# Optimization experiments

Measured on AMD Instinct MI355X. Metric: run time of the kernel, lower is better.

## Reference

```python
import jax, jax.numpy as jnp
import numpy as np

# dims: batch, seqlen, d_model, d_inner=2*d_model, d_state, dt_rank=ceil(dm/16), n_layer, vocab, d_conv
B_, L_, DM, DI, N, RK, NL, V, K = 2, 2048, 512, 1024, 16, 32, 4, 32000, 4


def setup_inputs() -> dict:
    key = jax.random.key(0)
    ks = jax.random.split(key, 10)
    s = lambda k, shape, scale: jax.random.normal(k, shape, jnp.float32) * scale
    return {
        "input_ids": jax.random.randint(ks[0], (B_, L_), 0, V),
        "emb": s(ks[1], (V, DM), 0.02),
        "in_proj_w": s(ks[2], (NL, 2 * DI, DM), DM ** -0.5),
        "conv_w": s(ks[3], (NL, DI, K), 0.2),
        "conv_b": jnp.zeros((NL, DI), jnp.float32),
        "x_proj_w": s(ks[4], (NL, RK + 2 * N, DI), DI ** -0.5),
        "dt_proj_w": s(ks[5], (NL, DI, RK), RK ** -0.5),
        "dt_proj_b": jnp.full((NL, DI), -4.6, jnp.float32),  # softplus^-1(~0.01)
        "A_log": jnp.tile(jnp.log(jnp.arange(1, N + 1, dtype=jnp.float32))[None, None, :], (NL, DI, 1)),
        "Dp": jnp.ones((NL, DI), jnp.float32),
        "out_proj_w": s(ks[6], (NL, DM, DI), DI ** -0.5),
        "norm_w": jnp.ones((NL, DM), jnp.float32),
        "norm_b": jnp.zeros((NL, DM), jnp.float32),
        "normf_w": jnp.ones((DM,), jnp.float32),
        "normf_b": jnp.zeros((DM,), jnp.float32),
        "dec_w": s(ks[7], (V, DM), DM ** -0.5),
        "dec_b": jnp.zeros((V,), jnp.float32),
    }


def layer_norm(x, w, b, eps=1e-5):
    m = x.mean(-1, keepdims=True)
    v = ((x - m) ** 2).mean(-1, keepdims=True)
    return (x - m) * jax.lax.rsqrt(v + eps) * w + b


def mamba_mixer(x, iw, cw, cb, xw, dw, db, A_log, Dv, ow):
    B, L, _ = x.shape
    xz = x @ iw.T                      # [B,L,2*DI]
    u, z = jnp.split(xz, 2, -1)
    # depthwise causal conv1d, kernel K
    up = jnp.pad(u, ((0, 0), (K - 1, 0), (0, 0)))
    u = sum(up[:, k:k + L, :] * cw[:, k] for k in range(K)) + cb
    u = jax.nn.silu(u)
    xdbl = u @ xw.T                    # [B,L,RK+2N]
    dt, Bm, Cm = jnp.split(xdbl, [RK, RK + N], -1)
    dt = jax.nn.softplus(dt @ dw.T + db)   # [B,L,DI]
    A = -jnp.exp(A_log)                    # [DI,N]
    dA = jnp.exp(dt[..., None] * A)                              # [B,L,DI,N]
    dBu = dt[..., None] * Bm[:, :, None, :] * u[..., None]       # [B,L,DI,N]

    def step(h, inp):
        dA_t, dBu_t, C_t = inp
        h = dA_t * h + dBu_t
        return h, jnp.einsum('bdn,bn->bd', h, C_t)

    h0 = jnp.zeros((B, DI, N), x.dtype)
    _, ys = jax.lax.scan(step, h0, (dA.transpose(1, 0, 2, 3), dBu.transpose(1, 0, 2, 3), Cm.transpose(1, 0, 2)))
    y = ys.transpose(1, 0, 2) + u * Dv
    y = y * jax.nn.silu(z)
    return y @ ow.T


def reference(input_ids, emb, in_proj_w, conv_w, conv_b, x_proj_w, dt_proj_w, dt_proj_b,
              A_log, Dp, out_proj_w, norm_w, norm_b, normf_w, normf_b, dec_w, dec_b):
    h = emb[input_ids]                 # [B,L,DM]
    residual = None
    for i in range(NL):
        residual = h + residual if residual is not None else h
        hn = layer_norm(residual, norm_w[i], norm_b[i])
        h = mamba_mixer(hn, in_proj_w[i], conv_w[i], conv_b[i], x_proj_w[i],
                        dt_proj_w[i], dt_proj_b[i], A_log[i], Dp[i], out_proj_w[i])
    residual = h + residual
    h = layer_norm(residual, normf_w, normf_b)
    return h @ dec_w.T + dec_b         # [B,L,V]
```

## Files before the change

kernel.cpp:

```cpp
#include <hip/hip_runtime.h>
#include <cstdint>
#include <cstddef>

typedef unsigned short u16;
typedef __attribute__((ext_vector_type(8))) short short8;
typedef __attribute__((ext_vector_type(4))) float f32x4;
typedef __attribute__((ext_vector_type(4))) unsigned short us4;

#define NB 2
#define SEQ 2048
#define DMODEL 512
#define DINNER 1024
#define NSTATE 16
#define RKK 32
#define NLAYER 4
#define VOCAB 32000
#define KCONV 4
#define MROWS 4096
#define NCHUNK 64
#define LCHUNK 32
#define XP_SPLITK 8
#define XP_KCH 128

#define GLOAD16(gp, lp) __builtin_amdgcn_global_load_lds( \
    (const __attribute__((address_space(1))) void*)(gp),  \
    (__attribute__((address_space(3))) void*)(lp), 16, 0, 0)

static __device__ __forceinline__ u16 f2bf(float f) {
  union { float f; uint32_t u; } v; v.f = f;
  uint32_t r = (v.u + 0x7FFFu + ((v.u >> 16) & 1u)) >> 16;
  return (u16)r;
}
static __device__ __forceinline__ float bf2f(u16 x) {
  union { uint32_t u; float f; } v; v.u = ((uint32_t)x) << 16; return v.f;
}

__global__ __launch_bounds__(256) void cvt_bf16_k(const float* __restrict__ s, u16* __restrict__ d, long n) {
  long i = ((long)blockIdx.x * 256 + threadIdx.x) * 4;
  if (i < n) {
    f32x4 v = *(const f32x4*)(s + i);
    us4 o; o.x = f2bf(v.x); o.y = f2bf(v.y); o.z = f2bf(v.z); o.w = f2bf(v.w);
    *(us4*)(d + i) = o;
  }
}
__global__ __launch_bounds__(256) void cvt_xproj_k(const float* __restrict__ s, u16* __restrict__ d) {
  long i = (long)blockIdx.x * 256 + threadIdx.x;
  int c = (int)(i & 1023); int r = ((int)(i >> 10)) & 127; int l = (int)(i >> 17);
  d[i] = (r < 64) ? f2bf(s[((long)l * 64 + r) * 1024 + c]) : (u16)0;
}

__global__ __launch_bounds__(256) void embed_k(const int* __restrict__ ids, const float* __restrict__ emb,
                        float* __restrict__ resid) {
  long gid = (long)blockIdx.x * 256 + threadIdx.x;
  int m = (int)(gid >> 9), c = (int)(gid & 511);
  resid[gid] = emb[(long)ids[m] * DMODEL + c];
}

__global__ __launch_bounds__(256) void ln_k(float* __restrict__ resid, const float* __restrict__ hadd,
                                            const float* __restrict__ w, const float* __restrict__ b,
                                            u16* __restrict__ obf) {
  int m = blockIdx.x, t = threadIdx.x;
  long base = (long)m * DMODEL;
  float x0 = resid[base + t], x1 = resid[base + t + 256];
  if (hadd) {
    x0 += hadd[base + t]; x1 += hadd[base + t + 256];
    resid[base + t] = x0; resid[base + t + 256] = x1;
  }
  float s = x0 + x1, q = x0 * x0 + x1 * x1;
  #pragma unroll
  for (int o = 1; o < 64; o <<= 1) { s += __shfl_xor(s, o, 64); q += __shfl_xor(q, o, 64); }
  __shared__ float ss[4], qq[4];
  int wv = t >> 6;
  if ((t & 63) == 0) { ss[wv] = s; qq[wv] = q; }
  __syncthreads();
  s = ss[0] + ss[1] + ss[2] + ss[3];
  q = qq[0] + qq[1] + qq[2] + qq[3];
  float mean = s * (1.f / DMODEL);
  float var = q * (1.f / DMODEL) - mean * mean;
  float rs = rsqrtf(var + 1e-5f);
  obf[base + t]       = f2bf((x0 - mean) * rs * w[t] + b[t]);
  obf[base + t + 256] = f2bf((x1 - mean) * rs * w[t + 256] + b[t + 256]);
}

__global__ __launch_bounds__(256) void conv_silu_k(const float* __restrict__ xz, const float* __restrict__ cw,
                            const float* __restrict__ cb, u16* __restrict__ ub) {
  int tid = blockIdx.x * 256 + threadIdx.x;
  int d = tid & (DINNER - 1);
  int g = tid >> 10;
  int m0 = g << 2;
  int t0 = m0 & (SEQ - 1);
  float w0 = cw[d * 4 + 0], w1 = cw[d * 4 + 1], w2 = cw[d * 4 + 2], w3 = cw[d * 4 + 3];
  float bias = cb[d];
  float v[7];
  #pragma unroll
  for (int j = 0; j < 7; ++j) {
    int tt = t0 + j - 3;
    v[j] = (tt >= 0) ? xz[(long)(m0 + j - 3) * (2 * DINNER) + d] : 0.f;
  }
  #pragma unroll
  for (int i = 0; i < 4; ++i) {
    float acc = bias + v[i] * w0 + v[i + 1] * w1 + v[i + 2] * w2 + v[i + 3] * w3;
    float sv = acc / (1.f + __expf(-acc));
    ub[(long)(m0 + i) * DINNER + d] = f2bf(sv);
  }
}

template <int EPI, bool SPLIT>
__global__ __launch_bounds__(256) void gemm_bf16(
    const u16* __restrict__ A, int lda, const u16* __restrict__ W, int ldw,
    float* __restrict__ C, u16* __restrict__ Cb, int ldc,
    const float* __restrict__ bias, int K, int kchunk, long zstride) {
  const int tid = threadIdx.x;
  const int nwg = gridDim.x * gridDim.y;
  const int wgid = blockIdx.y * gridDim.x + blockIdx.x;
  const int q = nwg >> 3;
  const int swz = (wgid & 7) * q + (wgid >> 3);
  const int bn = swz % gridDim.x, bm = swz / gridDim.x;
  int kb = 0, ke = K;
  if (SPLIT) { kb = blockIdx.z * kchunk; ke = kb + kchunk; C += (long)blockIdx.z * zstride; }
  const int wave = tid >> 6, lane = tid & 63;
  const int wm = (wave >> 1) * 64, wn = (wave & 1) * 64;
  __shared__ __align__(16) u16 sA[128 * 32];
  __shared__ __align__(16) u16 sB[128 * 32];
  f32x4 acc[4][4] = {};
  const long arow0 = (long)bm * 128, brow0 = (long)bn * 128;
  const int frow = lane & 15, fk = (lane >> 4) << 3;
  const int srow = lane >> 2, scol = (lane & 3) << 3;
  const int c0 = wave * 2;
  for (int k0 = kb; k0 < ke; k0 += 32) {
    __syncthreads();
    #pragma unroll
    for (int i = 0; i < 2; ++i) {
      int c = c0 + i;
      GLOAD16(A + (arow0 + 16 * c + srow) * (long)lda + k0 + scol, sA + c * 512);
      GLOAD16(W + (brow0 + 16 * c + srow) * (long)ldw + k0 + scol, sB + c * 512);
    }
    asm volatile("s_waitcnt vmcnt(0)" ::: "memory");
    __syncthreads();
    short8 aF[4], bF[4];
    #pragma unroll
    for (int i = 0; i < 4; ++i) aF[i] = *(const short8*)(sA + (wm + i * 16 + frow) * 32 + fk);
    #pragma unroll
    for (int i = 0; i < 4; ++i) bF[i] = *(const short8*)(sB + (wn + i * 16 + frow) * 32 + fk);
    #pragma unroll
    for (int mi = 0; mi < 4; ++mi)
      #pragma unroll
      for (int ni = 0; ni < 4; ++ni)
        acc[mi][ni] = __builtin_amdgcn_mfma_f32_16x16x32_bf16(aF[mi], bF[ni], acc[mi][ni], 0, 0, 0);
  }
  const int ccol = lane & 15, crow = (lane >> 4) << 2;
  #pragma unroll
  for (int mi = 0; mi < 4; ++mi) {
    #pragma unroll
    for (int ni = 0; ni < 4; ++ni) {
      long gr0 = arow0 + wm + mi * 16 + crow;
      long gc = brow0 + wn + ni * 16 + ccol;
      #pragma unroll
      for (int r = 0; r < 4; ++r) {
        float v = acc[mi][ni][r];
        long idx = (gr0 + r) * (long)ldc + gc;
        if (EPI == 0) {
          C[idx] = v;
        } else if (EPI == 1) {
          C[idx] = v; Cb[idx] = f2bf(v);
        } else if (EPI == 2) {
          float x = v + bias[gc];
          Cb[idx] = f2bf((x > 20.f) ? x : log1pf(__expf(x)));
        } else {
          C[idx] = v + bias[gc];
        }
      }
    }
  }
}

__global__ __launch_bounds__(256) void xp_comb_k(const float* __restrict__ P, float* __restrict__ xd,
                          u16* __restrict__ xdb) {
  long i = (long)blockIdx.x * 256 + threadIdx.x;
  float s = 0.f;
  #pragma unroll
  for (int z = 0; z < XP_SPLITK; ++z) s += P[(long)z * MROWS * 128 + i];
  xd[i] = s; xdb[i] = f2bf(s);
}

__global__ __launch_bounds__(256) void scanA_k(const u16* __restrict__ dtb, const u16* __restrict__ ubf,
                        const float* __restrict__ xd, const float* __restrict__ alog_l,
                        float* __restrict__ P, float* __restrict__ S) {
  int bid = blockIdx.x;
  int tid = threadIdx.x;
  int b = bid >> 8;
  int c = (bid >> 2) & (NCHUNK - 1);
  int d = ((bid & 3) << 8) + tid;
  long rbase = (long)(b * SEQ + c * LCHUNK);
  __shared__ __align__(16) float sB[LCHUNK][NSTATE];
  if (tid < 128) {
    int t = tid >> 2, k4 = (tid & 3) << 2;
    *(f32x4*)&sB[t][k4] = *(const f32x4*)(xd + (rbase + t) * 128 + RKK + k4);
  }
  u16 dtv[LCHUNK], uv[LCHUNK];
  const u16* dp = dtb + rbase * DINNER + d;
  const u16* up = ubf + rbase * DINNER + d;
  #pragma unroll
  for (int tt = 0; tt < LCHUNK; ++tt) { dtv[tt] = dp[(long)tt * DINNER]; uv[tt] = up[(long)tt * DINNER]; }
  float A[NSTATE], h[NSTATE], p[NSTATE];
  #pragma unroll
  for (int n4 = 0; n4 < 4; ++n4) {
    f32x4 a4 = *(const f32x4*)(alog_l + d * NSTATE + n4 * 4);
    #pragma unroll
    for (int j = 0; j < 4; ++j) { A[n4 * 4 + j] = -__expf(a4[j]); h[n4 * 4 + j] = 0.f; p[n4 * 4 + j] = 1.f; }
  }
  __syncthreads();
  #pragma unroll
  for (int tt = 0; tt < LCHUNK; ++tt) {
    float dv = bf2f(dtv[tt]);
    float du = dv * bf2f(uv[tt]);
    f32x4 b0 = *(const f32x4*)&sB[tt][0], b1 = *(const f32x4*)&sB[tt][4];
    f32x4 b2 = *(const f32x4*)&sB[tt][8], b3 = *(const f32x4*)&sB[tt][12];
    #pragma unroll
    for (int n = 0; n < NSTATE; ++n) {
      float dA = __expf(dv * A[n]);
      float bx = (n < 4) ? b0[n & 3] : (n < 8) ? b1[n & 3] : (n < 12) ? b2[n & 3] : b3[n & 3];
      h[n] = dA * h[n] + du * bx;
      p[n] *= dA;
    }
  }
  long base = (((long)(b * DINNER + d)) * NCHUNK + c) * NSTATE;
  #pragma unroll
  for (int n4 = 0; n4 < 4; ++n4) {
    f32x4 pv, sv;
    #pragma unroll
    for (int j = 0; j < 4; ++j) { pv[j] = p[n4 * 4 + j]; sv[j] = h[n4 * 4 + j]; }
    *(f32x4*)(P + base + n4 * 4) = pv;
    *(f32x4*)(S + base + n4 * 4) = sv;
  }
}

__global__ __launch_bounds__(256) void scanB_k(const float* __restrict__ P, const float* __restrict__ S,
                        float* __restrict__ Hin) {
  int w = blockIdx.x * 4 + (threadIdx.x >> 6);
  int lane = threadIdx.x & 63;
  long base = ((long)w * NCHUNK + lane) * NSTATE;
  float p[NSTATE], s[NSTATE];
  #pragma unroll
  for (int n = 0; n < NSTATE; ++n) { p[n] = P[base + n]; s[n] = S[base + n]; }
  #pragma unroll
  for (int off = 1; off < 64; off <<= 1) {
    float pp[NSTATE], sp[NSTATE];
    #pragma unroll
    for (int n = 0; n < NSTATE; ++n) {
      pp[n] = __shfl_up(p[n], off, 64);
      sp[n] = __shfl_up(s[n], off, 64);
    }
    if (lane >= off) {
      #pragma unroll
      for (int n = 0; n < NSTATE; ++n) { s[n] = p[n] * sp[n] + s[n]; p[n] *= pp[n]; }
    }
  }
  #pragma unroll
  for (int n = 0; n < NSTATE; ++n) {
    float hv = __shfl_up(s[n], 1, 64);
    Hin[base + n] = (lane == 0) ? 0.f : hv;
  }
}

__global__ __launch_bounds__(256) void scanC_k(const u16* __restrict__ dtb, const u16* __restrict__ ubf,
                        const float* __restrict__ xd, const float* __restrict__ alog_l,
                        const float* __restrict__ Dp_l, const float* __restrict__ xz,
                        const float* __restrict__ Hin, u16* __restrict__ ybf) {
  int bid = blockIdx.x;
  int tid = threadIdx.x;
  int b = bid >> 8;
  int c = (bid >> 2) & (NCHUNK - 1);
  int d = ((bid & 3) << 8) + tid;
  long rbase = (long)(b * SEQ + c * LCHUNK);
  __shared__ __align__(16) float sBC[LCHUNK][2 * NSTATE];
  {
    int t = tid >> 3, k4 = (tid & 7) << 2;
    *(f32x4*)&sBC[t][k4] = *(const f32x4*)(xd + (rbase + t) * 128 + RKK + k4);
  }
  u16 dtv[LCHUNK], uv[LCHUNK];
  float zv[LCHUNK];
  const u16* dp = dtb + rbase * DINNER + d;
  const u16* up = ubf + rbase * DINNER + d;
  const float* zp = xz + rbase * (2 * DINNER) + DINNER + d;
  #pragma unroll
  for (int tt = 0; tt < LCHUNK; ++tt) {
    dtv[tt] = dp[(long)tt * DINNER]; uv[tt] = up[(long)tt * DINNER];
    zv[tt] = zp[(long)tt * 2 * DINNER];
  }
  float A[NSTATE], h[NSTATE];
  long hbase = (((long)(b * DINNER + d)) * NCHUNK + c) * NSTATE;
  #pragma unroll
  for (int n4 = 0; n4 < 4; ++n4) {
    f32x4 a4 = *(const f32x4*)(alog_l + d * NSTATE + n4 * 4);
    f32x4 h4 = *(const f32x4*)(Hin + hbase + n4 * 4);
    #pragma unroll
    for (int j = 0; j < 4; ++j) { A[n4 * 4 + j] = -__expf(a4[j]); h[n4 * 4 + j] = h4[j]; }
  }
  float Dv = Dp_l[d];
  u16* yp = ybf + rbase * DINNER + d;
  __syncthreads();
  #pragma unroll
  for (int tt = 0; tt < LCHUNK; ++tt) {
    float dv = bf2f(dtv[tt]);
    float uvf = bf2f(uv[tt]);
    float du = dv * uvf;
    f32x4 b0 = *(const f32x4*)&sBC[tt][0], b1 = *(const f32x4*)&sBC[tt][4];
    f32x4 b2 = *(const f32x4*)&sBC[tt][8], b3 = *(const f32x4*)&sBC[tt][12];
    f32x4 c0 = *(const f32x4*)&sBC[tt][16], c1 = *(const f32x4*)&sBC[tt][20];
    f32x4 c2 = *(const f32x4*)&sBC[tt][24], c3 = *(const f32x4*)&sBC[tt][28];
    float y = 0.f;
    #pragma unroll
    for (int n = 0; n < NSTATE; ++n) {
      float dA = __expf(dv * A[n]);
      float bx = (n < 4) ? b0[n & 3] : (n < 8) ? b1[n & 3] : (n < 12) ? b2[n & 3] : b3[n & 3];
      float cx = (n < 4) ? c0[n & 3] : (n < 8) ? c1[n & 3] : (n < 12) ? c2[n & 3] : c3[n & 3];
      h[n] = dA * h[n] + du * bx;
      y += h[n] * cx;
    }
    y += uvf * Dv;
    float z = zv[tt];
    y *= z / (1.f + __expf(-z));
    yp[(long)tt * DINNER] = f2bf(y);
  }
}

extern "C" void kernel_launch(void* const* d_in, const int* in_sizes, int n_in,
                              void* d_out, int out_size, void* d_ws, size_t ws_size,
                              hipStream_t stream) {
  (void)in_sizes; (void)n_in; (void)out_size; (void)ws_size;
  const int*   ids = (const int*)d_in[0];
  const float* emb = (const float*)d_in[1];
  const float* ipw = (const float*)d_in[2];
  const float* cw  = (const float*)d_in[3];
  const float* cb  = (const float*)d_in[4];
  const float* xpw = (const float*)d_in[5];
  const float* dtw = (const float*)d_in[6];
  const float* dtb = (const float*)d_in[7];
  const float* alg = (const float*)d_in[8];
  const float* Dpp = (const float*)d_in[9];
  const float* opw = (const float*)d_in[10];
  const float* nw  = (const float*)d_in[11];
  const float* nb  = (const float*)d_in[12];
  const float* nfw = (const float*)d_in[13];
  const float* nfb = (const float*)d_in[14];
  const float* dw  = (const float*)d_in[15];
  const float* db  = (const float*)d_in[16];

  char* p = (char*)d_ws;
  auto carve = [&](size_t bytes) { void* r = (void*)p; p += (bytes + 255) & ~(size_t)255; return r; };
  float* resid  = (float*)carve((size_t)MROWS * DMODEL * 4);
  float* hmix   = (float*)carve((size_t)MROWS * DMODEL * 4);
  u16*   hnbf   = (u16*)  carve((size_t)MROWS * DMODEL * 2);
  u16*   hfbf   = (u16*)  carve((size_t)MROWS * DMODEL * 2);
  float* xz     = (float*)carve((size_t)MROWS * 2 * DINNER * 4);
  u16*   ubf    = (u16*)  carve((size_t)MROWS * DINNER * 2);
  float* xdbl   = (float*)carve((size_t)MROWS * 128 * 4);
  u16*   xdblbf = (u16*)  carve((size_t)MROWS * 128 * 2);
  float* xdP    = (float*)carve((size_t)XP_SPLITK * MROWS * 128 * 4);
  u16*   dtb16  = (u16*)  carve((size_t)MROWS * DINNER * 2);
  u16*   ybf    = (u16*)  carve((size_t)MROWS * DINNER * 2);
  float* chkP   = (float*)carve((size_t)NB * DINNER * NCHUNK * NSTATE * 4);
  float* chkS   = (float*)carve((size_t)NB * DINNER * NCHUNK * NSTATE * 4);
  float* hin    = (float*)carve((size_t)NB * DINNER * NCHUNK * NSTATE * 4);
  u16*   w_in   = (u16*)carve((size_t)NLAYER * 2 * DINNER * DMODEL * 2);
  u16*   w_xp   = (u16*)carve((size_t)NLAYER * 128 * DINNER * 2);
  u16*   w_dt   = (u16*)carve((size_t)NLAYER * DINNER * RKK * 2);
  u16*   w_out  = (u16*)carve((size_t)NLAYER * DMODEL * DINNER * 2);
  u16*   w_dec  = (u16*)carve((size_t)VOCAB * DMODEL * 2);

  {
    long n = (long)NLAYER * 2 * DINNER * DMODEL;
    cvt_bf16_k<<<(int)((n / 4 + 255) / 256), 256, 0, stream>>>(ipw, w_in, n);
    n = (long)NLAYER * DINNER * RKK;
    cvt_bf16_k<<<(int)((n / 4 + 255) / 256), 256, 0, stream>>>(dtw, w_dt, n);
    n = (long)NLAYER * DMODEL * DINNER;
    cvt_bf16_k<<<(int)((n / 4 + 255) / 256), 256, 0, stream>>>(opw, w_out, n);
    n = (long)VOCAB * DMODEL;
    cvt_bf16_k<<<(int)((n / 4 + 255) / 256), 256, 0, stream>>>(dw, w_dec, n);
    cvt_xproj_k<<<(NLAYER * 128 * DINNER) / 256, 256, 0, stream>>>(xpw, w_xp);
  }
  embed_k<<<(MROWS * DMODEL) / 256, 256, 0, stream>>>(ids, emb, resid);

  for (int i = 0; i < NLAYER; ++i) {
    ln_k<<<MROWS, 256, 0, stream>>>(resid, i ? hmix : nullptr, nw + i * DMODEL, nb + i * DMODEL, hnbf);
    gemm_bf16<0, false><<<dim3(2 * DINNER / 128, MROWS / 128), 256, 0, stream>>>(
        hnbf, DMODEL, w_in + (long)i * 2 * DINNER * DMODEL, DMODEL,
        xz, nullptr, 2 * DINNER, nullptr, DMODEL, 0, 0);
    conv_silu_k<<<(MROWS / 4 * DINNER) / 256, 256, 0, stream>>>(
        xz, cw + (long)i * DINNER * KCONV, cb + i * DINNER, ubf);
    gemm_bf16<0, true><<<dim3(1, MROWS / 128, XP_SPLITK), 256, 0, stream>>>(
        ubf, DINNER, w_xp + (long)i * 128 * DINNER, DINNER,
        xdP, nullptr, 128, nullptr, DINNER, XP_KCH, (long)MROWS * 128);
    xp_comb_k<<<(MROWS * 128) / 256, 256, 0, stream>>>(xdP, xdbl, xdblbf);
    gemm_bf16<2, false><<<dim3(DINNER / 128, MROWS / 128), 256, 0, stream>>>(
        xdblbf, 128, w_dt + (long)i * DINNER * RKK, RKK,
        nullptr, dtb16, DINNER, dtb + i * DINNER, RKK, 0, 0);
    scanA_k<<<NB * NCHUNK * 4, 256, 0, stream>>>(
        dtb16, ubf, xdbl, alg + (long)i * DINNER * NSTATE, chkP, chkS);
    scanB_k<<<(NB * DINNER) / 4, 256, 0, stream>>>(chkP, chkS, hin);
    scanC_k<<<NB * NCHUNK * 4, 256, 0, stream>>>(
        dtb16, ubf, xdbl, alg + (long)i * DINNER * NSTATE, Dpp + i * DINNER, xz, hin, ybf);
    gemm_bf16<0, false><<<dim3(DMODEL / 128, MROWS / 128), 256, 0, stream>>>(
        ybf, DINNER, w_out + (long)i * DMODEL * DINNER, DINNER,
        hmix, nullptr, DMODEL, nullptr, DINNER, 0, 0);
  }
  ln_k<<<MROWS, 256, 0, stream>>>(resid, hmix, nfw, nfb, hfbf);
  gemm_bf16<3, false><<<dim3(VOCAB / 128, MROWS / 128), 256, 0, stream>>>(
      hfbf, DMODEL, w_dec, DMODEL, (float*)d_out, nullptr, VOCAB, db, DMODEL, 0, 0);
}
```

Measured before the change: 930.2 us.

## Store in_proj output as bf16, deepen GEMM K-tile, fuse embed and weight conversions

After: 893.4 us. 1.04x faster.

```diff
diff --git a/kernel.cpp b/kernel.cpp
--- a/kernel.cpp
+++ b/kernel.cpp
@@ -15,7 +15,6 @@
 #define RKK 32
 #define NLAYER 4
 #define VOCAB 32000
-#define KCONV 4
 #define MROWS 4096
 #define NCHUNK 64
 #define LCHUNK 32
@@ -35,13 +34,25 @@
   union { uint32_t u; float f; } v; v.u = ((uint32_t)x) << 16; return v.f;
 }
 
-__global__ __launch_bounds__(256) void cvt_bf16_k(const float* __restrict__ s, u16* __restrict__ d, long n) {
-  long i = ((long)blockIdx.x * 256 + threadIdx.x) * 4;
-  if (i < n) {
-    f32x4 v = *(const f32x4*)(s + i);
-    us4 o; o.x = f2bf(v.x); o.y = f2bf(v.y); o.z = f2bf(v.z); o.w = f2bf(v.w);
-    *(us4*)(d + i) = o;
-  }
+__global__ __launch_bounds__(256) void cvt_all_k(
+    const float* __restrict__ ipw, const float* __restrict__ dtw,
+    const float* __restrict__ opw, const float* __restrict__ dw,
+    u16* __restrict__ w_in, u16* __restrict__ w_dt,
+    u16* __restrict__ w_out, u16* __restrict__ w_dec) {
+  const long n0 = (long)NLAYER * 2 * DINNER * DMODEL / 4;
+  const long n1 = (long)NLAYER * DINNER * RKK / 4;
+  const long n2 = (long)NLAYER * DMODEL * DINNER / 4;
+  const long n3 = (long)VOCAB * DMODEL / 4;
+  long i = (long)blockIdx.x * 256 + threadIdx.x;
+  const float* s; u16* d; long off;
+  if (i < n0) { s = ipw; d = w_in; off = i; }
+  else if (i < n0 + n1) { s = dtw; d = w_dt; off = i - n0; }
+  else if (i < n0 + n1 + n2) { s = opw; d = w_out; off = i - n0 - n1; }
+  else if (i < n0 + n1 + n2 + n3) { s = dw; d = w_dec; off = i - n0 - n1 - n2; }
+  else return;
+  f32x4 v = *(const f32x4*)(s + off * 4);
+  us4 o; o.x = f2bf(v.x); o.y = f2bf(v.y); o.z = f2bf(v.z); o.w = f2bf(v.w);
+  *(us4*)(d + off * 4) = o;
 }
 __global__ __launch_bounds__(256) void cvt_xproj_k(const float* __restrict__ s, u16* __restrict__ d) {
   long i = (long)blockIdx.x * 256 + threadIdx.x;
@@ -49,21 +60,21 @@
   d[i] = (r < 64) ? f2bf(s[((long)l * 64 + r) * 1024 + c]) : (u16)0;
 }
 
-__global__ __launch_bounds__(256) void embed_k(const int* __restrict__ ids, const float* __restrict__ emb,
-                        float* __restrict__ resid) {
-  long gid = (long)blockIdx.x * 256 + threadIdx.x;
-  int m = (int)(gid >> 9), c = (int)(gid & 511);
-  resid[gid] = emb[(long)ids[m] * DMODEL + c];
-}
-
-__global__ __launch_bounds__(256) void ln_k(float* __restrict__ resid, const float* __restrict__ hadd,
+template <int MODE>
+__global__ __launch_bounds__(256) void ln_k(const int* __restrict__ ids, const float* __restrict__ emb,
+                                            float* __restrict__ resid, const float* __restrict__ hadd,
                                             const float* __restrict__ w, const float* __restrict__ b,
                                             u16* __restrict__ obf) {
   int m = blockIdx.x, t = threadIdx.x;
   long base = (long)m * DMODEL;
-  float x0 = resid[base + t], x1 = resid[base + t + 256];
-  if (hadd) {
-    x0 += hadd[base + t]; x1 += hadd[base + t + 256];
+  float x0, x1;
+  if (MODE == 0) {
+    long ebase = (long)ids[m] * DMODEL;
+    x0 = emb[ebase + t]; x1 = emb[ebase + t + 256];
+    resid[base + t] = x0; resid[base + t + 256] = x1;
+  } else {
+    x0 = resid[base + t] + hadd[base + t];
+    x1 = resid[base + t + 256] + hadd[base + t + 256];
     resid[base + t] = x0; resid[base + t + 256] = x1;
   }
   float s = x0 + x1, q = x0 * x0 + x1 * x1;
@@ -82,7 +93,7 @@
   obf[base + t + 256] = f2bf((x1 - mean) * rs * w[t + 256] + b[t + 256]);
 }
 
-__global__ __launch_bounds__(256) void conv_silu_k(const float* __restrict__ xz, const float* __restrict__ cw,
+__global__ __launch_bounds__(256) void conv_silu_k(const u16* __restrict__ xzb, const float* __restrict__ cw,
                             const float* __restrict__ cb, u16* __restrict__ ub) {
   int tid = blockIdx.x * 256 + threadIdx.x;
   int d = tid & (DINNER - 1);
@@ -95,7 +106,7 @@
   #pragma unroll
   for (int j = 0; j < 7; ++j) {
     int tt = t0 + j - 3;
-    v[j] = (tt >= 0) ? xz[(long)(m0 + j - 3) * (2 * DINNER) + d] : 0.f;
+    v[j] = (tt >= 0) ? bf2f(xzb[(long)(m0 + j - 3) * (2 * DINNER) + d]) : 0.f;
   }
   #pragma unroll
   for (int i = 0; i < 4; ++i) {
@@ -105,7 +116,7 @@
   }
 }
 
-template <int EPI, bool SPLIT>
+template <int EPI, int BK, bool SPLIT>
 __global__ __launch_bounds__(256) void gemm_bf16(
     const u16* __restrict__ A, int lda, const u16* __restrict__ W, int ldw,
     float* __restrict__ C, u16* __restrict__ Cb, int ldc,
@@ -120,33 +131,45 @@
   if (SPLIT) { kb = blockIdx.z * kchunk; ke = kb + kchunk; C += (long)blockIdx.z * zstride; }
   const int wave = tid >> 6, lane = tid & 63;
   const int wm = (wave >> 1) * 64, wn = (wave & 1) * 64;
-  __shared__ __align__(16) u16 sA[128 * 32];
-  __shared__ __align__(16) u16 sB[128 * 32];
+  __shared__ __align__(16) u16 sA[128 * BK];
+  __shared__ __align__(16) u16 sB[128 * BK];
   f32x4 acc[4][4] = {};
   const long arow0 = (long)bm * 128, brow0 = (long)bn * 128;
   const int frow = lane & 15, fk = (lane >> 4) << 3;
-  const int srow = lane >> 2, scol = (lane & 3) << 3;
-  const int c0 = wave * 2;
-  for (int k0 = kb; k0 < ke; k0 += 32) {
+  for (int k0 = kb; k0 < ke; k0 += BK) {
     __syncthreads();
-    #pragma unroll
-    for (int i = 0; i < 2; ++i) {
-      int c = c0 + i;
-      GLOAD16(A + (arow0 + 16 * c + srow) * (long)lda + k0 + scol, sA + c * 512);
-      GLOAD16(W + (brow0 + 16 * c + srow) * (long)ldw + k0 + scol, sB + c * 512);
+    if (BK == 32) {
+      const int srow = lane >> 2, scol = (lane & 3) << 3;
+      #pragma unroll
+      for (int i = 0; i < 2; ++i) {
+        int c = wave * 2 + i;
+        GLOAD16(A + (arow0 + 16 * c + srow) * (long)lda + k0 + scol, sA + c * 512);
+        GLOAD16(W + (brow0 + 16 * c + srow) * (long)ldw + k0 + scol, sB + c * 512);
+      }
+    } else {
+      const int srow = lane >> 3, scol = (lane & 7) << 3;
+      #pragma unroll
+      for (int i = 0; i < 4; ++i) {
+        int c = wave * 4 + i;
+        GLOAD16(A + (arow0 + 8 * c + srow) * (long)lda + k0 + scol, sA + c * 512);
+        GLOAD16(W + (brow0 + 8 * c + srow) * (long)ldw + k0 + scol, sB + c * 512);
+      }
     }
     asm volatile("s_waitcnt vmcnt(0)" ::: "memory");
     __syncthreads();
-    short8 aF[4], bF[4];
-    #pragma unroll
-    for (int i = 0; i < 4; ++i) aF[i] = *(const short8*)(sA + (wm + i * 16 + frow) * 32 + fk);
-    #pragma unroll
-    for (int i = 0; i < 4; ++i) bF[i] = *(const short8*)(sB + (wn + i * 16 + frow) * 32 + fk);
-    #pragma unroll
-    for (int mi = 0; mi < 4; ++mi)
-      #pragma unroll
-      for (int ni = 0; ni < 4; ++ni)
-        acc[mi][ni] = __builtin_amdgcn_mfma_f32_16x16x32_bf16(aF[mi], bF[ni], acc[mi][ni], 0, 0, 0);
+    #pragma unroll
+    for (int ks = 0; ks < BK / 32; ++ks) {
+      short8 aF[4], bF[4];
+      #pragma unroll
+      for (int i = 0; i < 4; ++i) aF[i] = *(const short8*)(sA + (wm + i * 16 + frow) * BK + ks * 32 + fk);
+      #pragma unroll
+      for (int i = 0; i < 4; ++i) bF[i] = *(const short8*)(sB + (wn + i * 16 + frow) * BK + ks * 32 + fk);
+      #pragma unroll
+      for (int mi = 0; mi < 4; ++mi)
+        #pragma unroll
+        for (int ni = 0; ni < 4; ++ni)
+          acc[mi][ni] = __builtin_amdgcn_mfma_f32_16x16x32_bf16(aF[mi], bF[ni], acc[mi][ni], 0, 0, 0);
+    }
   }
   const int ccol = lane & 15, crow = (lane >> 4) << 2;
   #pragma unroll
@@ -162,12 +185,12 @@
         if (EPI == 0) {
           C[idx] = v;
         } else if (EPI == 1) {
-          C[idx] = v; Cb[idx] = f2bf(v);
+          Cb[idx] = f2bf(v);
         } else if (EPI == 2) {
           float x = v + bias[gc];
           Cb[idx] = f2bf((x > 20.f) ? x : log1pf(__expf(x)));
         } else {
-          C[idx] = v + bias[gc];
+          __builtin_nontemporal_store(v + bias[gc], &C[idx]);
         }
       }
     }
@@ -265,7 +288,7 @@
 
 __global__ __launch_bounds__(256) void scanC_k(const u16* __restrict__ dtb, const u16* __restrict__ ubf,
                         const float* __restrict__ xd, const float* __restrict__ alog_l,
-                        const float* __restrict__ Dp_l, const float* __restrict__ xz,
+                        const float* __restrict__ Dp_l, const u16* __restrict__ xzb,
                         const float* __restrict__ Hin, u16* __restrict__ ybf) {
   int bid = blockIdx.x;
   int tid = threadIdx.x;
@@ -278,11 +301,10 @@
     int t = tid >> 3, k4 = (tid & 7) << 2;
     *(f32x4*)&sBC[t][k4] = *(const f32x4*)(xd + (rbase + t) * 128 + RKK + k4);
   }
-  u16 dtv[LCHUNK], uv[LCHUNK];
-  float zv[LCHUNK];
+  u16 dtv[LCHUNK], uv[LCHUNK], zv[LCHUNK];
   const u16* dp = dtb + rbase * DINNER + d;
   const u16* up = ubf + rbase * DINNER + d;
-  const float* zp = xz + rbase * (2 * DINNER) + DINNER + d;
+  const u16* zp = xzb + rbase * (2 * DINNER) + DINNER + d;
   #pragma unroll
   for (int tt = 0; tt < LCHUNK; ++tt) {
     dtv[tt] = dp[(long)tt * DINNER]; uv[tt] = up[(long)tt * DINNER];
@@ -319,7 +341,7 @@
       y += h[n] * cx;
     }
     y += uvf * Dv;
-    float z = zv[tt];
+    float z = bf2f(zv[tt]);
     y *= z / (1.f + __expf(-z));
     yp[(long)tt * DINNER] = f2bf(y);
   }
@@ -353,7 +375,7 @@
   float* hmix   = (float*)carve((size_t)MROWS * DMODEL * 4);
   u16*   hnbf   = (u16*)  carve((size_t)MROWS * DMODEL * 2);
   u16*   hfbf   = (u16*)  carve((size_t)MROWS * DMODEL * 2);
-  float* xz     = (float*)carve((size_t)MROWS * 2 * DINNER * 4);
+  u16*   xzb    = (u16*)  carve((size_t)MROWS * 2 * DINNER * 2);
   u16*   ubf    = (u16*)  carve((size_t)MROWS * DINNER * 2);
   float* xdbl   = (float*)carve((size_t)MROWS * 128 * 4);
   u16*   xdblbf = (u16*)  carve((size_t)MROWS * 128 * 2);
@@ -370,42 +392,39 @@
   u16*   w_dec  = (u16*)carve((size_t)VOCAB * DMODEL * 2);
 
   {
-    long n = (long)NLAYER * 2 * DINNER * DMODEL;
-    cvt_bf16_k<<<(int)((n / 4 + 255) / 256), 256, 0, stream>>>(ipw, w_in, n);
-    n = (long)NLAYER * DINNER * RKK;
-    cvt_bf16_k<<<(int)((n / 4 + 255) / 256), 256, 0, stream>>>(dtw, w_dt, n);
-    n = (long)NLAYER * DMODEL * DINNER;
-    cvt_bf16_k<<<(int)((n / 4 + 255) / 256), 256, 0, stream>>>(opw, w_out, n);
-    n = (long)VOCAB * DMODEL;
-    cvt_bf16_k<<<(int)((n / 4 + 255) / 256), 256, 0, stream>>>(dw, w_dec, n);
+    long nv4 = ((long)NLAYER * 2 * DINNER * DMODEL + (long)NLAYER * DINNER * RKK +
+                (long)NLAYER * DMODEL * DINNER + (long)VOCAB * DMODEL) / 4;
+    cvt_all_k<<<(int)((nv4 + 255) / 256), 256, 0, stream>>>(ipw, dtw, opw, dw, w_in, w_dt, w_out, w_dec);
     cvt_xproj_k<<<(NLAYER * 128 * DINNER) / 256, 256, 0, stream>>>(xpw, w_xp);
   }
-  embed_k<<<(MROWS * DMODEL) / 256, 256, 0, stream>>>(ids, emb, resid);
 
   for (int i = 0; i < NLAYER; ++i) {
-    ln_k<<<MROWS, 256, 0, stream>>>(resid, i ? hmix : nullptr, nw + i * DMODEL, nb + i * DMODEL, hnbf);
-    gemm_bf16<0, false><<<dim3(2 * DINNER / 128, MROWS / 128), 256, 0, stream>>>(
+    if (i == 0)
+      ln_k<0><<<MROWS, 256, 0, stream>>>(ids, emb, resid, nullptr, nw, nb, hnbf);
+    else
+      ln_k<1><<<MROWS, 256, 0, stream>>>(nullptr, nullptr, resid, hmix, nw + i * DMODEL, nb + i * DMODEL, hnbf);
+    gemm_bf16<1, 64, false><<<dim3(2 * DINNER / 128, MROWS / 128), 256, 0, stream>>>(
         hnbf, DMODEL, w_in + (long)i * 2 * DINNER * DMODEL, DMODEL,
-        xz, nullptr, 2 * DINNER, nullptr, DMODEL, 0, 0);
+        nullptr, xzb, 2 * DINNER, nullptr, DMODEL, 0, 0);
     conv_silu_k<<<(MROWS / 4 * DINNER) / 256, 256, 0, stream>>>(
-        xz, cw + (long)i * DINNER * KCONV, cb + i * DINNER, ubf);
-    gemm_bf16<0, true><<<dim3(1, MROWS / 128, XP_SPLITK), 256, 0, stream>>>(
+        xzb, cw + (long)i * DINNER * 4, cb + i * DINNER, ubf);
+    gemm_bf16<0, 64, true><<<dim3(1, MROWS / 128, XP_SPLITK), 256, 0, stream>>>(
         ubf, DINNER, w_xp + (long)i * 128 * DINNER, DINNER,
         xdP, nullptr, 128, nullptr, DINNER, XP_KCH, (long)MROWS * 128);
     xp_comb_k<<<(MROWS * 128) / 256, 256, 0, stream>>>(xdP, xdbl, xdblbf);
-    gemm_bf16<2, false><<<dim3(DINNER / 128, MROWS / 128), 256, 0, stream>>>(
+    gemm_bf16<2, 32, false><<<dim3(DINNER / 128, MROWS / 128), 256, 0, stream>>>(
         xdblbf, 128, w_dt + (long)i * DINNER * RKK, RKK,
         nullptr, dtb16, DINNER, dtb + i * DINNER, RKK, 0, 0);
     scanA_k<<<NB * NCHUNK * 4, 256, 0, stream>>>(
         dtb16, ubf, xdbl, alg + (long)i * DINNER * NSTATE, chkP, chkS);
     scanB_k<<<(NB * DINNER) / 4, 256, 0, stream>>>(chkP, chkS, hin);
     scanC_k<<<NB * NCHUNK * 4, 256, 0, stream>>>(
-        dtb16, ubf, xdbl, alg + (long)i * DINNER * NSTATE, Dpp + i * DINNER, xz, hin, ybf);
-    gemm_bf16<0, false><<<dim3(DMODEL / 128, MROWS / 128), 256, 0, stream>>>(
+        dtb16, ubf, xdbl, alg + (long)i * DINNER * NSTATE, Dpp + i * DINNER, xzb, hin, ybf);
+    gemm_bf16<0, 64, false><<<dim3(DMODEL / 128, MROWS / 128), 256, 0, stream>>>(
         ybf, DINNER, w_out + (long)i * DMODEL * DINNER, DINNER,
         hmix, nullptr, DMODEL, nullptr, DINNER, 0, 0);
   }
-  ln_k<<<MROWS, 256, 0, stream>>>(resid, hmix, nfw, nfb, hfbf);
-  gemm_bf16<3, false><<<dim3(VOCAB / 128, MROWS / 128), 256, 0, stream>>>(
+  ln_k<1><<<MROWS, 256, 0, stream>>>(nullptr, nullptr, resid, hmix, nfw, nfb, hfbf);
+  gemm_bf16<3, 64, false><<<dim3(VOCAB / 128, MROWS / 128), 256, 0, stream>>>(
       hfbf, DMODEL, w_dec, DMODEL, (float*)d_out, nullptr, VOCAB, db, DMODEL, 0, 0);
 }
```
